# Performance work log

Measured on AMD Instinct MI355X. Metric: run time of the kernel, lower is better.

## Reference

```python
import jax, jax.numpy as jnp
import numpy as np

N = 50000
E = 600000
P = 100000
IN_FEATS = 128
HIDDEN = 128


def _glorot(key, shape):
    fan_in, fan_out = shape[0], shape[1]
    lim = np.sqrt(6.0 / (fan_in + fan_out)).astype(np.float32)
    return jax.random.uniform(key, shape, jnp.float32, -lim, lim)


def setup_inputs() -> dict:
    key = jax.random.key(0)
    ks = jax.random.split(key, 20)
    inp = {
        "x": jax.random.normal(ks[0], (N, IN_FEATS), jnp.float32),
        "edge_src": jax.random.randint(ks[1], (E,), 0, N, jnp.int32),
        "edge_dst": jax.random.randint(ks[2], (E,), 0, N, jnp.int32),
        "pos_src": jax.random.randint(ks[3], (P,), 0, N, jnp.int32),
        "pos_dst": jax.random.randint(ks[4], (P,), 0, N, jnp.int32),
        "neg_src": jax.random.randint(ks[5], (P,), 0, N, jnp.int32),
        "neg_dst": jax.random.randint(ks[6], (P,), 0, N, jnp.int32),
        # SAGEConv layer 1 (in_feats -> hidden)
        "Ws1": _glorot(ks[7], (IN_FEATS, HIDDEN)),
        "Wn1": _glorot(ks[8], (IN_FEATS, HIDDEN)),
        "b1": jnp.zeros((HIDDEN,), jnp.float32),
        # SAGEConv layer 2 (hidden -> hidden)
        "Ws2": _glorot(ks[9], (HIDDEN, HIDDEN)),
        "Wn2": _glorot(ks[10], (HIDDEN, HIDDEN)),
        "b2": jnp.zeros((HIDDEN,), jnp.float32),
        # EdgeDecoder MLP: Linear-ReLU-Linear-ReLU-Linear(->1)
        "Wd1": _glorot(ks[11], (HIDDEN, HIDDEN)),
        "bd1": jnp.zeros((HIDDEN,), jnp.float32),
        "Wd2": _glorot(ks[12], (HIDDEN, HIDDEN)),
        "bd2": jnp.zeros((HIDDEN,), jnp.float32),
        "Wd3": _glorot(ks[13], (HIDDEN, 1)),
        "bd3": jnp.zeros((1,), jnp.float32),
    }
    return inp


def _sage_conv(h, src, dst, Ws, Wn, b):
    # mean aggregation over incoming neighbors, then fc_self + fc_neigh + bias
    msg = h[src]                                             # [E, d]
    agg = jax.ops.segment_sum(msg, dst, num_segments=N)      # [N, d]
    deg = jax.ops.segment_sum(jnp.ones((src.shape[0],), h.dtype), dst,
                              num_segments=N)
    mean = agg / jnp.maximum(deg, 1.0)[:, None]
    return h @ Ws + mean @ Wn + b


def _decode(h, src, dst, Wd1, bd1, Wd2, bd2, Wd3, bd3):
    z = h[src] * h[dst]                                      # [P, d]
    z = jax.nn.relu(z @ Wd1 + bd1)
    z = jax.nn.relu(z @ Wd2 + bd2)
    return z @ Wd3 + bd3                                     # [P, 1]


def reference(x, edge_src, edge_dst, pos_src, pos_dst, neg_src, neg_dst,
              Ws1, Wn1, b1, Ws2, Wn2, b2, Wd1, bd1, Wd2, bd2, Wd3, bd3):
    h = jax.nn.relu(_sage_conv(x, edge_src, edge_dst, Ws1, Wn1, b1))
    h = _sage_conv(h, edge_src, edge_dst, Ws2, Wn2, b2)  # last layer: no act
    h_pos = _decode(h, pos_src, pos_dst, Wd1, bd1, Wd2, bd2, Wd3, bd3)
    h_neg = _decode(h, neg_src, neg_dst, Wd1, bd1, Wd2, bd2, Wd3, bd3)
    return (h_pos, h_neg)
```

## Files before the change

kernel.cpp:

```cpp
#include <hip/hip_runtime.h>
#include <hip/hip_bf16.h>

#define N_NODES 50000
#define N_EDGES 600000
#define N_PAIRS 100000

typedef __attribute__((ext_vector_type(8))) short bf16x8;
typedef __attribute__((ext_vector_type(4))) float f32x4;

__device__ inline unsigned short f2b(float f) {
    unsigned u = __float_as_uint(f);
    unsigned r = u + 0x7fff + ((u >> 16) & 1);
    return (unsigned short)(r >> 16);
}
__device__ inline float b2f(unsigned short h) {
    return __uint_as_float(((unsigned)h) << 16);
}

__global__ void k_convert_x(const float* __restrict__ x, unsigned short* __restrict__ A1,
                            unsigned short* __restrict__ xb16,
                            const int* __restrict__ edge_dst, int* __restrict__ deg) {
    int idx = blockIdx.x * blockDim.x + threadIdx.x;
    if (idx < N_EDGES) atomicAdd(&deg[edge_dst[idx]], 1);
    if (idx >= N_NODES * 32) return;
    int row = idx >> 5, c4 = (idx & 31) * 4;
    float4 v = *(const float4*)(x + row * 128 + c4);
    unsigned lo = (unsigned)f2b(v.x) | ((unsigned)f2b(v.y) << 16);
    unsigned hi = (unsigned)f2b(v.z) | ((unsigned)f2b(v.w) << 16);
    uint2 o; o.x = lo; o.y = hi;
    *(uint2*)(A1 + row * 256 + c4) = o;
    *(uint2*)(xb16 + row * 128 + c4) = o;
}

__global__ void k_prep_w(const float* __restrict__ Ws1, const float* __restrict__ Wn1,
                         const float* __restrict__ Ws2, const float* __restrict__ Wn2,
                         const float* __restrict__ Wd1, const float* __restrict__ Wd2,
                         unsigned short* __restrict__ WT1, unsigned short* __restrict__ WT2,
                         unsigned short* __restrict__ WdT1, unsigned short* __restrict__ WdT2) {
    int id = blockIdx.x * blockDim.x + threadIdx.x;
    if (id < 32768) {
        int j = id & 7, g = id >> 3;
        int lane = g & 63, t = g >> 6;
        int ct = t & 7, kb = t >> 3;
        int k = kb * 32 + (lane >> 4) * 8 + j, n = ct * 16 + (lane & 15);
        float v = (k < 128) ? Ws1[k * 128 + n] : Wn1[(k - 128) * 128 + n];
        WT1[id] = f2b(v);
    } else if (id < 65536) {
        int r = id - 32768;
        int j = r & 7, g = r >> 3;
        int lane = g & 63, t = g >> 6;
        int ct = t & 7, kb = t >> 3;
        int k = kb * 32 + (lane >> 4) * 8 + j, n = ct * 16 + (lane & 15);
        float v = (k < 128) ? Ws2[k * 128 + n] : Wn2[(k - 128) * 128 + n];
        WT2[r] = f2b(v);
    } else if (id < 81920) {
        int r = id - 65536;
        int j = r & 7, g = r >> 3;
        int lane = g & 63, t = g >> 6;
        int ct = t & 7, kb = t >> 3;
        int k = kb * 32 + (lane >> 4) * 8 + j, n = ct * 16 + (lane & 15);
        WdT1[r] = f2b(Wd1[k * 128 + n]);
    } else if (id < 98304) {
        int r = id - 81920;
        int j = r & 7, g = r >> 3;
        int lane = g & 63, t = g >> 6;
        int ct = t & 7, kb = t >> 3;
        int k = kb * 32 + (lane >> 4) * 8 + j, n = ct * 16 + (lane & 15);
        WdT2[r] = f2b(Wd2[k * 128 + n]);
    }
}

__global__ void k_scan1(const int* __restrict__ deg, int* __restrict__ row_ptr,
                        int* __restrict__ bsum, int n) {
    __shared__ int tmp[1024];
    int i = blockIdx.x * 1024 + threadIdx.x;
    int d = (i < n) ? deg[i] : 0;
    tmp[threadIdx.x] = d;
    __syncthreads();
    int run = d;
    for (int off = 1; off < 1024; off <<= 1) {
        int t = (threadIdx.x >= off) ? tmp[threadIdx.x - off] : 0;
        __syncthreads();
        run += t;
        tmp[threadIdx.x] = run;
        __syncthreads();
    }
    if (i < n) row_ptr[i] = run - d;
    if (threadIdx.x == 1023) bsum[blockIdx.x] = run;
}

__global__ void k_add(int* __restrict__ row_ptr, int* __restrict__ cursor,
                      const int* __restrict__ bsum, int n) {
    __shared__ int prefix;
    if (threadIdx.x == 0) {
        int acc = 0;
        for (int j = 0; j < (int)blockIdx.x; j++) acc += bsum[j];
        prefix = acc;
    }
    __syncthreads();
    int i = blockIdx.x * 1024 + threadIdx.x;
    if (i < n) {
        int v = row_ptr[i] + prefix;
        row_ptr[i] = v;
        cursor[i] = v;
    }
    if (i == 0) row_ptr[n] = N_EDGES;
}

__global__ void k_scatter(const int* __restrict__ src, const int* __restrict__ dst,
                          int* __restrict__ cursor, int* __restrict__ colA) {
    int e = blockIdx.x * blockDim.x + threadIdx.x;
    if (e < N_EDGES) {
        int d = dst[e];
        int slot = atomicAdd(&cursor[d], 1);
        colA[slot] = src[e];
    }
}

__global__ __launch_bounds__(256) void k_agg(const unsigned short* __restrict__ hb, int ldh,
                                             const int* __restrict__ row_ptr,
                                             const int* __restrict__ colA,
                                             unsigned short* __restrict__ outm, int ldo) {
    int wave = (blockIdx.x * blockDim.x + threadIdx.x) >> 6;
    int lane = threadIdx.x & 63;
    int q = lane >> 4, ql = lane & 15;
    int w = wave * 4 + q;
    if (w >= N_NODES) w = N_NODES - 1;
    int s = row_ptr[w], e = row_ptr[w + 1];
    float a[8];
#pragma unroll
    for (int j = 0; j < 8; j++) a[j] = 0.f;
    for (int base = s; base < e; base += 16) {
        int ce = (base + ql < e) ? colA[base + ql] : 0;
        int cnt = min(16, e - base);
        int ei[16];
#pragma unroll
        for (int j = 0; j < 16; j++) {
            int sl = (j < cnt) ? j : (cnt - 1);
            ei[j] = __shfl(ce, (q << 4) + sl, 64);
        }
        uint4 v[16];
#pragma unroll
        for (int j = 0; j < 16; j++)
            v[j] = *(const uint4*)(hb + (size_t)ei[j] * ldh + ql * 8);
#pragma unroll
        for (int j = 0; j < 16; j += 2) {
            const unsigned* p0 = (const unsigned*)&v[j];
            const unsigned* p1 = (const unsigned*)&v[j + 1];
            if (j + 1 < cnt) {
#pragma unroll
                for (int t = 0; t < 4; t++) {
                    a[2 * t] += b2f(p0[t] & 0xffff) + b2f(p1[t] & 0xffff);
                    a[2 * t + 1] += b2f(p0[t] >> 16) + b2f(p1[t] >> 16);
                }
            } else if (j < cnt) {
#pragma unroll
                for (int t = 0; t < 4; t++) {
                    a[2 * t] += b2f(p0[t] & 0xffff);
                    a[2 * t + 1] += b2f(p0[t] >> 16);
                }
            }
        }
    }
    float rd = 1.0f / (float)max(e - s, 1);
    uint4 o;
    unsigned* op = (unsigned*)&o;
#pragma unroll
    for (int t = 0; t < 4; t++)
        op[t] = (unsigned)f2b(a[2 * t] * rd) | ((unsigned)f2b(a[2 * t + 1] * rd) << 16);
    *(uint4*)(outm + (size_t)w * ldo + ql * 8) = o;
}

__global__ __launch_bounds__(256) void k_gemm(const unsigned short* __restrict__ A, int lda, int K,
                                              const unsigned short* __restrict__ BT,
                                              const float* __restrict__ bias,
                                              unsigned short* __restrict__ Hout, int ldo,
                                              int M, int relu) {
    int wv = threadIdx.x >> 6, lane = threadIdx.x & 63;
    int lr = lane & 15, lq = lane >> 4;
    int r0 = blockIdx.x * 128 + wv * 32;
    int arow0 = min(r0 + lr, M - 1);
    int arow1 = min(r0 + 16 + lr, M - 1);
    f32x4 acc[2][8];
    f32x4 zero = {0.f, 0.f, 0.f, 0.f};
#pragma unroll
    for (int m = 0; m < 2; m++)
#pragma unroll
        for (int ct = 0; ct < 8; ct++) acc[m][ct] = zero;
    for (int kb = 0; kb < K; kb += 32) {
        int ka = kb + lq * 8;
        int kbi = kb >> 5;
        bf16x8 wf[8];
#pragma unroll
        for (int ct = 0; ct < 8; ct++)
            wf[ct] = *(const bf16x8*)(BT + ((size_t)(kbi * 8 + ct) * 64 + lane) * 8);
        bf16x8 af0 = *(const bf16x8*)(A + (size_t)arow0 * lda + ka);
        bf16x8 af1 = *(const bf16x8*)(A + (size_t)arow1 * lda + ka);
#pragma unroll
        for (int ct = 0; ct < 8; ct++) {
            acc[0][ct] = __builtin_amdgcn_mfma_f32_16x16x32_bf16(af0, wf[ct], acc[0][ct], 0, 0, 0);
            acc[1][ct] = __builtin_amdgcn_mfma_f32_16x16x32_bf16(af1, wf[ct], acc[1][ct], 0, 0, 0);
        }
    }
#pragma unroll
    for (int m = 0; m < 2; m++) {
#pragma unroll
        for (int ct = 0; ct < 8; ct++) {
            int colc = ct * 16 + lr;
            float bv = bias[colc];
#pragma unroll
            for (int r = 0; r < 4; r++) {
                int row = r0 + m * 16 + lq * 4 + r;
                if (row < M) {
                    float v = acc[m][ct][r] + bv;
                    if (relu) v = fmaxf(v, 0.f);
                    Hout[(size_t)row * ldo + colc] = f2b(v);
                }
            }
        }
    }
}

__global__ __launch_bounds__(64) void k_mlp(const unsigned short* __restrict__ h2b,
                                            const int* __restrict__ pos_src,
                                            const int* __restrict__ pos_dst,
                                            const int* __restrict__ neg_src,
                                            const int* __restrict__ neg_dst,
                                            const unsigned short* __restrict__ WdT1,
                                            const unsigned short* __restrict__ WdT2,
                                            const float* __restrict__ bd1,
                                            const float* __restrict__ bd2,
                                            const float* __restrict__ Wd3,
                                            const float* __restrict__ bd3,
                                            float* __restrict__ out, int P2) {
    __shared__ unsigned short t1[32][136];
    const int lane = threadIdx.x & 63, lr = lane & 15, lq = lane >> 4;
    const int row0 = blockIdx.x * 32;
    int p0 = min(row0 + lr, P2 - 1);
    int p1 = min(row0 + 16 + lr, P2 - 1);
    int s0i = (p0 < N_PAIRS) ? pos_src[p0] : neg_src[p0 - N_PAIRS];
    int d0i = (p0 < N_PAIRS) ? pos_dst[p0] : neg_dst[p0 - N_PAIRS];
    int s1i = (p1 < N_PAIRS) ? pos_src[p1] : neg_src[p1 - N_PAIRS];
    int d1i = (p1 < N_PAIRS) ? pos_dst[p1] : neg_dst[p1 - N_PAIRS];
    uint4 za0[4], zb0[4], za1[4], zb1[4];
#pragma unroll
    for (int kb = 0; kb < 4; kb++) {
        int ka = kb * 32 + lq * 8;
        za0[kb] = *(const uint4*)(h2b + (size_t)s0i * 128 + ka);
        zb0[kb] = *(const uint4*)(h2b + (size_t)d0i * 128 + ka);
        za1[kb] = *(const uint4*)(h2b + (size_t)s1i * 128 + ka);
        zb1[kb] = *(const uint4*)(h2b + (size_t)d1i * 128 + ka);
    }
    bf16x8 af0[4], af1[4];
#pragma unroll
    for (int kb = 0; kb < 4; kb++) {
        unsigned r0v[4], r1v[4];
        const unsigned* a0p = (const unsigned*)&za0[kb];
        const unsigned* b0p = (const unsigned*)&zb0[kb];
        const unsigned* a1p = (const unsigned*)&za1[kb];
        const unsigned* b1p = (const unsigned*)&zb1[kb];
#pragma unroll
        for (int j = 0; j < 4; j++) {
            unsigned short lo0 = f2b(b2f(a0p[j] & 0xffff) * b2f(b0p[j] & 0xffff));
            unsigned short hi0 = f2b(b2f(a0p[j] >> 16) * b2f(b0p[j] >> 16));
            r0v[j] = (unsigned)lo0 | ((unsigned)hi0 << 16);
            unsigned short lo1 = f2b(b2f(a1p[j] & 0xffff) * b2f(b1p[j] & 0xffff));
            unsigned short hi1 = f2b(b2f(a1p[j] >> 16) * b2f(b1p[j] >> 16));
            r1v[j] = (unsigned)lo1 | ((unsigned)hi1 << 16);
        }
        af0[kb] = *(const bf16x8*)r0v;
        af1[kb] = *(const bf16x8*)r1v;
    }
    f32x4 zero = {0.f, 0.f, 0.f, 0.f};
    f32x4 acc[2][8];
#pragma unroll
    for (int m = 0; m < 2; m++)
#pragma unroll
        for (int ct = 0; ct < 8; ct++) acc[m][ct] = zero;
#pragma unroll
    for (int kb = 0; kb < 4; kb++) {
        bf16x8 wf[8];
#pragma unroll
        for (int ct = 0; ct < 8; ct++)
            wf[ct] = *(const bf16x8*)(WdT1 + ((size_t)(kb * 8 + ct) * 64 + lane) * 8);
#pragma unroll
        for (int ct = 0; ct < 8; ct++) {
            acc[0][ct] = __builtin_amdgcn_mfma_f32_16x16x32_bf16(af0[kb], wf[ct], acc[0][ct], 0, 0, 0);
            acc[1][ct] = __builtin_amdgcn_mfma_f32_16x16x32_bf16(af1[kb], wf[ct], acc[1][ct], 0, 0, 0);
        }
    }
#pragma unroll
    for (int m = 0; m < 2; m++)
#pragma unroll
        for (int ct = 0; ct < 8; ct++) {
            int colc = ct * 16 + lr;
            float bv = bd1[colc];
#pragma unroll
            for (int r = 0; r < 4; r++) {
                float v = fmaxf(acc[m][ct][r] + bv, 0.f);
                t1[m * 16 + lq * 4 + r][colc] = f2b(v);
            }
        }
    __syncthreads();
#pragma unroll
    for (int m = 0; m < 2; m++)
#pragma unroll
        for (int ct = 0; ct < 8; ct++) acc[m][ct] = zero;
#pragma unroll
    for (int kb = 0; kb < 4; kb++) {
        int ka = kb * 32 + lq * 8;
        bf16x8 wf[8];
#pragma unroll
        for (int ct = 0; ct < 8; ct++)
            wf[ct] = *(const bf16x8*)(WdT2 + ((size_t)(kb * 8 + ct) * 64 + lane) * 8);
        bf16x8 bf0 = *(const bf16x8*)(&t1[lr][ka]);
        bf16x8 bf1 = *(const bf16x8*)(&t1[16 + lr][ka]);
#pragma unroll
        for (int ct = 0; ct < 8; ct++) {
            acc[0][ct] = __builtin_amdgcn_mfma_f32_16x16x32_bf16(bf0, wf[ct], acc[0][ct], 0, 0, 0);
            acc[1][ct] = __builtin_amdgcn_mfma_f32_16x16x32_bf16(bf1, wf[ct], acc[1][ct], 0, 0, 0);
        }
    }
    float sc[2][4] = {{0.f, 0.f, 0.f, 0.f}, {0.f, 0.f, 0.f, 0.f}};
#pragma unroll
    for (int ct = 0; ct < 8; ct++) {
        int colc = ct * 16 + lr;
        float bv = bd2[colc];
        float w3 = Wd3[colc];
#pragma unroll
        for (int m = 0; m < 2; m++)
#pragma unroll
            for (int r = 0; r < 4; r++) {
                float v = fmaxf(acc[m][ct][r] + bv, 0.f);
                sc[m][r] += v * w3;
            }
    }
#pragma unroll
    for (int mm = 1; mm < 16; mm <<= 1)
#pragma unroll
        for (int m = 0; m < 2; m++)
#pragma unroll
            for (int r = 0; r < 4; r++) sc[m][r] += __shfl_xor(sc[m][r], mm, 64);
    if (lr == 0) {
        float b3 = bd3[0];
#pragma unroll
        for (int m = 0; m < 2; m++)
#pragma unroll
            for (int r = 0; r < 4; r++) {
                int g = row0 + m * 16 + lq * 4 + r;
                if (g < P2) out[g] = sc[m][r] + b3;
            }
    }
}

static inline size_t alignup(size_t v) { return (v + 255) & ~(size_t)255; }

extern "C" void kernel_launch(void* const* d_in, const int* in_sizes, int n_in,
                              void* d_out, int out_size, void* d_ws, size_t ws_size,
                              hipStream_t stream) {
    const float* x = (const float*)d_in[0];
    const int* edge_src = (const int*)d_in[1];
    const int* edge_dst = (const int*)d_in[2];
    const int* pos_src = (const int*)d_in[3];
    const int* pos_dst = (const int*)d_in[4];
    const int* neg_src = (const int*)d_in[5];
    const int* neg_dst = (const int*)d_in[6];
    const float* Ws1 = (const float*)d_in[7];
    const float* Wn1 = (const float*)d_in[8];
    const float* b1 = (const float*)d_in[9];
    const float* Ws2 = (const float*)d_in[10];
    const float* Wn2 = (const float*)d_in[11];
    const float* b2 = (const float*)d_in[12];
    const float* Wd1 = (const float*)d_in[13];
    const float* bd1 = (const float*)d_in[14];
    const float* Wd2 = (const float*)d_in[15];
    const float* bd2 = (const float*)d_in[16];
    const float* Wd3 = (const float*)d_in[17];
    const float* bd3 = (const float*)d_in[18];
    float* out = (float*)d_out;

    char* p = (char*)d_ws;
    int* deg = (int*)p;            p += alignup(N_NODES * 4);
    int* row_ptr = (int*)p;        p += alignup((N_NODES + 1) * 4);
    int* cursor = (int*)p;         p += alignup(N_NODES * 4);
    int* bsum = (int*)p;           p += alignup(64 * 4);
    int* colA = (int*)p;           p += alignup(N_EDGES * 4);
    unsigned short* A1 = (unsigned short*)p;  p += alignup((size_t)N_NODES * 256 * 2);
    unsigned short* A2 = (unsigned short*)p;  p += alignup((size_t)N_NODES * 256 * 2);
    unsigned short* h2b = (unsigned short*)p; p += alignup((size_t)N_NODES * 128 * 2);
    unsigned short* WT1 = (unsigned short*)p;  p += alignup(32768 * 2);
    unsigned short* WT2 = (unsigned short*)p;  p += alignup(32768 * 2);
    unsigned short* WdT1 = (unsigned short*)p; p += alignup(16384 * 2);
    unsigned short* WdT2 = (unsigned short*)p; p += alignup(16384 * 2);
    unsigned short* xb16 = h2b;

    hipMemsetAsync(deg, 0, N_NODES * 4, stream);

    k_convert_x<<<(N_NODES * 32 + 255) / 256, 256, 0, stream>>>(x, A1, xb16, edge_dst, deg);
    k_prep_w<<<384, 256, 0, stream>>>(Ws1, Wn1, Ws2, Wn2, Wd1, Wd2, WT1, WT2, WdT1, WdT2);

    int nb1 = (N_NODES + 1023) / 1024;
    k_scan1<<<nb1, 1024, 0, stream>>>(deg, row_ptr, bsum, N_NODES);
    k_add<<<nb1, 1024, 0, stream>>>(row_ptr, cursor, bsum, N_NODES);
    k_scatter<<<(N_EDGES + 255) / 256, 256, 0, stream>>>(edge_src, edge_dst, cursor, colA);

    int nagg = (N_NODES + 15) / 16;

    k_agg<<<nagg, 256, 0, stream>>>(xb16, 128, row_ptr, colA, A1 + 128, 256);
    k_gemm<<<(N_NODES + 127) / 128, 256, 0, stream>>>(A1, 256, 256, WT1, b1, A2, 256, N_NODES, 1);

    k_agg<<<nagg, 256, 0, stream>>>(A2, 256, row_ptr, colA, A2 + 128, 256);
    k_gemm<<<(N_NODES + 127) / 128, 256, 0, stream>>>(A2, 256, 256, WT2, b2, h2b, 128, N_NODES, 0);

    k_mlp<<<(N_PAIRS * 2 + 31) / 32, 64, 0, stream>>>(h2b, pos_src, pos_dst, neg_src, neg_dst,
                                                      WdT1, WdT2, bd1, bd2, Wd3, bd3,
                                                      out, N_PAIRS * 2);
}
```

Before: 297.1 us.

## Make decoder MLP persistent with LDS-resident weights and per-wave tiles

The decoder MLP kernel becomes a persistent grid of 256 blocks of 512 threads. Each block loads both decoder weight matrices into shared memory once, then each wave loops over 32-pair tiles using its own slice of the intermediate buffer. This replaces repeated global/L2 weight fetches per small block with LDS reads and swaps the block barrier for a per-wave LDS wait. It costs a large shared-memory footprint (about 130 KB), which limits occupancy, and leaves less parallelism to hide the latency of the gathers.

```diff
diff --git a/kernel.cpp b/kernel.cpp
--- a/kernel.cpp
+++ b/kernel.cpp
@@ -221,135 +221,154 @@
     }
 }
 
-__global__ __launch_bounds__(64) void k_mlp(const unsigned short* __restrict__ h2b,
-                                            const int* __restrict__ pos_src,
-                                            const int* __restrict__ pos_dst,
-                                            const int* __restrict__ neg_src,
-                                            const int* __restrict__ neg_dst,
-                                            const unsigned short* __restrict__ WdT1,
-                                            const unsigned short* __restrict__ WdT2,
-                                            const float* __restrict__ bd1,
-                                            const float* __restrict__ bd2,
-                                            const float* __restrict__ Wd3,
-                                            const float* __restrict__ bd3,
-                                            float* __restrict__ out, int P2) {
-    __shared__ unsigned short t1[32][136];
-    const int lane = threadIdx.x & 63, lr = lane & 15, lq = lane >> 4;
-    const int row0 = blockIdx.x * 32;
-    int p0 = min(row0 + lr, P2 - 1);
-    int p1 = min(row0 + 16 + lr, P2 - 1);
-    int s0i = (p0 < N_PAIRS) ? pos_src[p0] : neg_src[p0 - N_PAIRS];
-    int d0i = (p0 < N_PAIRS) ? pos_dst[p0] : neg_dst[p0 - N_PAIRS];
-    int s1i = (p1 < N_PAIRS) ? pos_src[p1] : neg_src[p1 - N_PAIRS];
-    int d1i = (p1 < N_PAIRS) ? pos_dst[p1] : neg_dst[p1 - N_PAIRS];
-    uint4 za0[4], zb0[4], za1[4], zb1[4];
-#pragma unroll
-    for (int kb = 0; kb < 4; kb++) {
-        int ka = kb * 32 + lq * 8;
-        za0[kb] = *(const uint4*)(h2b + (size_t)s0i * 128 + ka);
-        zb0[kb] = *(const uint4*)(h2b + (size_t)d0i * 128 + ka);
-        za1[kb] = *(const uint4*)(h2b + (size_t)s1i * 128 + ka);
-        zb1[kb] = *(const uint4*)(h2b + (size_t)d1i * 128 + ka);
-    }
-    bf16x8 af0[4], af1[4];
-#pragma unroll
-    for (int kb = 0; kb < 4; kb++) {
-        unsigned r0v[4], r1v[4];
-        const unsigned* a0p = (const unsigned*)&za0[kb];
-        const unsigned* b0p = (const unsigned*)&zb0[kb];
-        const unsigned* a1p = (const unsigned*)&za1[kb];
-        const unsigned* b1p = (const unsigned*)&zb1[kb];
-#pragma unroll
-        for (int j = 0; j < 4; j++) {
-            unsigned short lo0 = f2b(b2f(a0p[j] & 0xffff) * b2f(b0p[j] & 0xffff));
-            unsigned short hi0 = f2b(b2f(a0p[j] >> 16) * b2f(b0p[j] >> 16));
-            r0v[j] = (unsigned)lo0 | ((unsigned)hi0 << 16);
-            unsigned short lo1 = f2b(b2f(a1p[j] & 0xffff) * b2f(b1p[j] & 0xffff));
-            unsigned short hi1 = f2b(b2f(a1p[j] >> 16) * b2f(b1p[j] >> 16));
-            r1v[j] = (unsigned)lo1 | ((unsigned)hi1 << 16);
-        }
-        af0[kb] = *(const bf16x8*)r0v;
-        af1[kb] = *(const bf16x8*)r1v;
-    }
-    f32x4 zero = {0.f, 0.f, 0.f, 0.f};
-    f32x4 acc[2][8];
-#pragma unroll
-    for (int m = 0; m < 2; m++)
-#pragma unroll
-        for (int ct = 0; ct < 8; ct++) acc[m][ct] = zero;
-#pragma unroll
-    for (int kb = 0; kb < 4; kb++) {
-        bf16x8 wf[8];
-#pragma unroll
-        for (int ct = 0; ct < 8; ct++)
-            wf[ct] = *(const bf16x8*)(WdT1 + ((size_t)(kb * 8 + ct) * 64 + lane) * 8);
-#pragma unroll
-        for (int ct = 0; ct < 8; ct++) {
-            acc[0][ct] = __builtin_amdgcn_mfma_f32_16x16x32_bf16(af0[kb], wf[ct], acc[0][ct], 0, 0, 0);
-            acc[1][ct] = __builtin_amdgcn_mfma_f32_16x16x32_bf16(af1[kb], wf[ct], acc[1][ct], 0, 0, 0);
-        }
-    }
-#pragma unroll
-    for (int m = 0; m < 2; m++)
+__global__ __launch_bounds__(512) void k_mlp(const unsigned short* __restrict__ h2b,
+                                             const int* __restrict__ pos_src,
+                                             const int* __restrict__ pos_dst,
+                                             const int* __restrict__ neg_src,
+                                             const int* __restrict__ neg_dst,
+                                             const unsigned short* __restrict__ WdT1,
+                                             const unsigned short* __restrict__ WdT2,
+                                             const float* __restrict__ bd1,
+                                             const float* __restrict__ bd2,
+                                             const float* __restrict__ Wd3,
+                                             const float* __restrict__ bd3,
+                                             float* __restrict__ out, int P2) {
+    __shared__ unsigned short wds[32768];
+    __shared__ unsigned short t1[8][32][136];
+    const int tid = threadIdx.x;
+    {
+        const uint4* s1 = (const uint4*)WdT1;
+        const uint4* s2 = (const uint4*)WdT2;
+        uint4* d = (uint4*)wds;
+#pragma unroll
+        for (int i = 0; i < 4; i++) d[tid + i * 512] = s1[tid + i * 512];
+#pragma unroll
+        for (int i = 0; i < 4; i++) d[2048 + tid + i * 512] = s2[tid + i * 512];
+    }
+    __syncthreads();
+    const unsigned short* wd1 = wds;
+    const unsigned short* wd2 = wds + 16384;
+    const int wv = tid >> 6;
+    const int lane = tid & 63, lr = lane & 15, lq = lane >> 4;
+    const int nw = gridDim.x << 3;
+    const int nt = P2 >> 5;
+    for (int tile = blockIdx.x * 8 + wv; tile < nt; tile += nw) {
+        const int row0 = tile * 32;
+        int p0 = min(row0 + lr, P2 - 1);
+        int p1 = min(row0 + 16 + lr, P2 - 1);
+        int s0i = (p0 < N_PAIRS) ? pos_src[p0] : neg_src[p0 - N_PAIRS];
+        int d0i = (p0 < N_PAIRS) ? pos_dst[p0] : neg_dst[p0 - N_PAIRS];
+        int s1i = (p1 < N_PAIRS) ? pos_src[p1] : neg_src[p1 - N_PAIRS];
+        int d1i = (p1 < N_PAIRS) ? pos_dst[p1] : neg_dst[p1 - N_PAIRS];
+        uint4 za0[4], zb0[4], za1[4], zb1[4];
+#pragma unroll
+        for (int kb = 0; kb < 4; kb++) {
+            int ka = kb * 32 + lq * 8;
+            za0[kb] = *(const uint4*)(h2b + (size_t)s0i * 128 + ka);
+            zb0[kb] = *(const uint4*)(h2b + (size_t)d0i * 128 + ka);
+            za1[kb] = *(const uint4*)(h2b + (size_t)s1i * 128 + ka);
+            zb1[kb] = *(const uint4*)(h2b + (size_t)d1i * 128 + ka);
+        }
+        bf16x8 af0[4], af1[4];
+#pragma unroll
+        for (int kb = 0; kb < 4; kb++) {
+            unsigned r0v[4], r1v[4];
+            const unsigned* a0p = (const unsigned*)&za0[kb];
+            const unsigned* b0p = (const unsigned*)&zb0[kb];
+            const unsigned* a1p = (const unsigned*)&za1[kb];
+            const unsigned* b1p = (const unsigned*)&zb1[kb];
+#pragma unroll
+            for (int j = 0; j < 4; j++) {
+                unsigned short lo0 = f2b(b2f(a0p[j] & 0xffff) * b2f(b0p[j] & 0xffff));
+                unsigned short hi0 = f2b(b2f(a0p[j] >> 16) * b2f(b0p[j] >> 16));
+                r0v[j] = (unsigned)lo0 | ((unsigned)hi0 << 16);
+                unsigned short lo1 = f2b(b2f(a1p[j] & 0xffff) * b2f(b1p[j] & 0xffff));
+                unsigned short hi1 = f2b(b2f(a1p[j] >> 16) * b2f(b1p[j] >> 16));
+                r1v[j] = (unsigned)lo1 | ((unsigned)hi1 << 16);
+            }
+            af0[kb] = *(const bf16x8*)r0v;
+            af1[kb] = *(const bf16x8*)r1v;
+        }
+        f32x4 zero = {0.f, 0.f, 0.f, 0.f};
+        f32x4 acc[2][8];
+#pragma unroll
+        for (int m = 0; m < 2; m++)
+#pragma unroll
+            for (int ct = 0; ct < 8; ct++) acc[m][ct] = zero;
+#pragma unroll
+        for (int kb = 0; kb < 4; kb++) {
+            bf16x8 wf[8];
+#pragma unroll
+            for (int ct = 0; ct < 8; ct++)
+                wf[ct] = *(const bf16x8*)(wd1 + ((kb * 8 + ct) * 64 + lane) * 8);
+#pragma unroll
+            for (int ct = 0; ct < 8; ct++) {
+                acc[0][ct] = __builtin_amdgcn_mfma_f32_16x16x32_bf16(af0[kb], wf[ct], acc[0][ct], 0, 0, 0);
+                acc[1][ct] = __builtin_amdgcn_mfma_f32_16x16x32_bf16(af1[kb], wf[ct], acc[1][ct], 0, 0, 0);
+            }
+        }
+#pragma unroll
+        for (int m = 0; m < 2; m++)
+#pragma unroll
+            for (int ct = 0; ct < 8; ct++) {
+                int colc = ct * 16 + lr;
+                float bv = bd1[colc];
+#pragma unroll
+                for (int r = 0; r < 4; r++) {
+                    float v = fmaxf(acc[m][ct][r] + bv, 0.f);
+                    t1[wv][m * 16 + lq * 4 + r][colc] = f2b(v);
+                }
+            }
+        asm volatile("s_waitcnt lgkmcnt(0)" ::: "memory");
+#pragma unroll
+        for (int m = 0; m < 2; m++)
+#pragma unroll
+            for (int ct = 0; ct < 8; ct++) acc[m][ct] = zero;
+#pragma unroll
+        for (int kb = 0; kb < 4; kb++) {
+            int ka = kb * 32 + lq * 8;
+            bf16x8 wf[8];
+#pragma unroll
+            for (int ct = 0; ct < 8; ct++)
+                wf[ct] = *(const bf16x8*)(wd2 + ((kb * 8 + ct) * 64 + lane) * 8);
+            bf16x8 bf0 = *(const bf16x8*)(&t1[wv][lr][ka]);
+            bf16x8 bf1 = *(const bf16x8*)(&t1[wv][16 + lr][ka]);
+#pragma unroll
+            for (int ct = 0; ct < 8; ct++) {
+                acc[0][ct] = __builtin_amdgcn_mfma_f32_16x16x32_bf16(bf0, wf[ct], acc[0][ct], 0, 0, 0);
+                acc[1][ct] = __builtin_amdgcn_mfma_f32_16x16x32_bf16(bf1, wf[ct], acc[1][ct], 0, 0, 0);
+            }
+        }
+        float sc[2][4] = {{0.f, 0.f, 0.f, 0.f}, {0.f, 0.f, 0.f, 0.f}};
 #pragma unroll
         for (int ct = 0; ct < 8; ct++) {
             int colc = ct * 16 + lr;
-            float bv = bd1[colc];
-#pragma unroll
-            for (int r = 0; r < 4; r++) {
-                float v = fmaxf(acc[m][ct][r] + bv, 0.f);
-                t1[m * 16 + lq * 4 + r][colc] = f2b(v);
-            }
-        }
-    __syncthreads();
-#pragma unroll
-    for (int m = 0; m < 2; m++)
-#pragma unroll
-        for (int ct = 0; ct < 8; ct++) acc[m][ct] = zero;
-#pragma unroll
-    for (int kb = 0; kb < 4; kb++) {
-        int ka = kb * 32 + lq * 8;
-        bf16x8 wf[8];
-#pragma unroll
-        for (int ct = 0; ct < 8; ct++)
-            wf[ct] = *(const bf16x8*)(WdT2 + ((size_t)(kb * 8 + ct) * 64 + lane) * 8);
-        bf16x8 bf0 = *(const bf16x8*)(&t1[lr][ka]);
-        bf16x8 bf1 = *(const bf16x8*)(&t1[16 + lr][ka]);
-#pragma unroll
-        for (int ct = 0; ct < 8; ct++) {
-            acc[0][ct] = __builtin_amdgcn_mfma_f32_16x16x32_bf16(bf0, wf[ct], acc[0][ct], 0, 0, 0);
-            acc[1][ct] = __builtin_amdgcn_mfma_f32_16x16x32_bf16(bf1, wf[ct], acc[1][ct], 0, 0, 0);
-        }
-    }
-    float sc[2][4] = {{0.f, 0.f, 0.f, 0.f}, {0.f, 0.f, 0.f, 0.f}};
-#pragma unroll
-    for (int ct = 0; ct < 8; ct++) {
-        int colc = ct * 16 + lr;
-        float bv = bd2[colc];
-        float w3 = Wd3[colc];
-#pragma unroll
-        for (int m = 0; m < 2; m++)
-#pragma unroll
-            for (int r = 0; r < 4; r++) {
-                float v = fmaxf(acc[m][ct][r] + bv, 0.f);
-                sc[m][r] += v * w3;
-            }
-    }
-#pragma unroll
-    for (int mm = 1; mm < 16; mm <<= 1)
-#pragma unroll
-        for (int m = 0; m < 2; m++)
-#pragma unroll
-            for (int r = 0; r < 4; r++) sc[m][r] += __shfl_xor(sc[m][r], mm, 64);
-    if (lr == 0) {
-        float b3 = bd3[0];
-#pragma unroll
-        for (int m = 0; m < 2; m++)
-#pragma unroll
-            for (int r = 0; r < 4; r++) {
-                int g = row0 + m * 16 + lq * 4 + r;
-                if (g < P2) out[g] = sc[m][r] + b3;
-            }
+            float bv = bd2[colc];
+            float w3 = Wd3[colc];
+#pragma unroll
+            for (int m = 0; m < 2; m++)
+#pragma unroll
+                for (int r = 0; r < 4; r++) {
+                    float v = fmaxf(acc[m][ct][r] + bv, 0.f);
+                    sc[m][r] += v * w3;
+                }
+        }
+#pragma unroll
+        for (int mm = 1; mm < 16; mm <<= 1)
+#pragma unroll
+            for (int m = 0; m < 2; m++)
+#pragma unroll
+                for (int r = 0; r < 4; r++) sc[m][r] += __shfl_xor(sc[m][r], mm, 64);
+        if (lr == 0) {
+            float b3 = bd3[0];
+#pragma unroll
+            for (int m = 0; m < 2; m++)
+#pragma unroll
+                for (int r = 0; r < 4; r++) {
+                    int g = row0 + m * 16 + lq * 4 + r;
+                    if (g < P2) out[g] = sc[m][r] + b3;
+                }
+        }
     }
 }
 
@@ -412,7 +431,7 @@
     k_agg<<<nagg, 256, 0, stream>>>(A2, 256, row_ptr, colA, A2 + 128, 256);
     k_gemm<<<(N_NODES + 127) / 128, 256, 0, stream>>>(A2, 256, 256, WT2, b2, h2b, 128, N_NODES, 0);
 
-    k_mlp<<<(N_PAIRS * 2 + 31) / 32, 64, 0, stream>>>(h2b, pos_src, pos_dst, neg_src, neg_dst,
-                                                      WdT1, WdT2, bd1, bd2, Wd3, bd3,
-                                                      out, N_PAIRS * 2);
-}
+    k_mlp<<<256, 512, 0, stream>>>(h2b, pos_src, pos_dst, neg_src, neg_dst,
+                                   WdT1, WdT2, bd1, bd2, Wd3, bd3,
+                                   out, N_PAIRS * 2);
+}
```

New measurement: 287.0 us. 3.4% less time.
